# Performance work log

Hardware: AMD Instinct MI355X
Metric: run time of the kernel (lower is better)

## Reference

```python
import jax, jax.numpy as jnp
import numpy as np

B, TQ, TK, DQ, DK, DV = 16, 1024, 1024, 1024, 1024, 1024


def setup_inputs() -> dict:
    key = jax.random.key(0)
    k1, k2, k3, k4, k5 = jax.random.split(key, 5)
    query = jax.random.normal(k1, (B, TQ, DQ), dtype=jnp.float32)
    keys = jax.random.normal(k2, (B, TK, DK), dtype=jnp.float32)
    values = jax.random.normal(k3, (B, TK, DV), dtype=jnp.float32)
    W = jax.random.normal(k4, (DQ, DK), dtype=jnp.float32) / np.sqrt(DQ)
    mask = jax.random.normal(k5, (B, TK), dtype=jnp.float32)
    return {"query": query, "keys": keys, "values": values, "W": W, "mask": mask}


def reference(query, keys, values, W, mask):
    # Bilinear (Luong 'general') score: weight[b,q,k] = query[b,q,:] @ W @ keys[b,k,:]
    qW = jnp.einsum('bqd,de->bqe', query, W)              # [B, Tq, Dk]
    weight = jnp.einsum('bqe,bke->bqk', qW, keys)         # [B, Tq, Tk]
    weight = weight + mask[:, None, :]                    # additive mask, broadcast over Tq
    score = jax.nn.softmax(weight, axis=-1)               # [B, Tq, Tk]
    ctx = jnp.einsum('bqk,bkv->bqv', score, values)       # [B, Tq, Dv]
    return (score, ctx)
```

## Files before the change

### kernel.cpp

```cpp
#include <hip/hip_runtime.h>
#include <hip/hip_bf16.h>

typedef _Float16 f16;
typedef __attribute__((ext_vector_type(8))) _Float16 half8;
typedef __attribute__((ext_vector_type(4))) float f32x4;

#define BM 256
#define BN 256
#define BK 64

__device__ __forceinline__ void gl2lds16(const f16* g, const f16* l) {
    __builtin_amdgcn_global_load_lds(
        (const __attribute__((address_space(1))) unsigned int*)g,
        (__attribute__((address_space(3))) unsigned int*)l, 16, 0, 0);
}

#define MFMA(d, a, b) d = __builtin_amdgcn_mfma_f32_16x16x32_f16(a, b, d, 0, 0, 0)

__global__ __launch_bounds__(256)
void cast_f16(const float* __restrict__ in, f16* __restrict__ out, long long n) {
    long long i = ((long long)blockIdx.x * 256 + threadIdx.x) * 8;
    if (i >= n) return;
    float4 a = *(const float4*)&in[i];
    float4 b = *(const float4*)&in[i + 4];
    union { f16 h[8]; uint4 q; } H;
    H.h[0] = (f16)a.x; H.h[1] = (f16)a.y; H.h[2] = (f16)a.z; H.h[3] = (f16)a.w;
    H.h[4] = (f16)b.x; H.h[5] = (f16)b.y; H.h[6] = (f16)b.z; H.h[7] = (f16)b.w;
    *(uint4*)&out[i] = H.q;
}

__global__ __launch_bounds__(256)
void transpose_f16(const float* __restrict__ in, f16* __restrict__ out,
                   int R, int C, long long in_stride, long long out_stride) {
    const int b = blockIdx.z;
    in += (size_t)b * in_stride;
    out += (size_t)b * out_stride;

    __shared__ float tile[32][33];
    const int r0 = blockIdx.y * 32, c0 = blockIdx.x * 32;
    const int t = threadIdx.x;
    const int tr = t >> 5, tc = t & 31;
    for (int i = 0; i < 4; i++)
        tile[tr + i * 8][tc] = in[(size_t)(r0 + tr + i * 8) * C + c0 + tc];
    __syncthreads();
    for (int i = 0; i < 4; i++) {
        float v = tile[tc][tr + i * 8];
        out[(size_t)(c0 + tr + i * 8) * R + r0 + tc] = (f16)v;
    }
}

template<int EPI>
__global__ __launch_bounds__(512, 2)
void gemm256(const f16* __restrict__ A_, const f16* __restrict__ B_,
             float* __restrict__ Cf, f16* __restrict__ Ch,
             const float* __restrict__ mask,
             int M, int N, int K,
             long long batchA, long long batchB, long long batchC) {
    const int b = blockIdx.z;
    const int m0 = blockIdx.y * BM;
    const int n0 = blockIdx.x * BN;
    const int t = threadIdx.x;
    const int lane = t & 63, wv = t >> 6;
    const int wr = wv >> 2;
    const int wc = wv & 3;

    const f16* A = A_ + (size_t)b * batchA;
    const f16* B = B_ + (size_t)b * batchB;

    __shared__ alignas(16) f16 sA[2][2][128][64];
    __shared__ alignas(16) f16 sB[2][2][128][64];

    const int srow  = wv * 16 + (lane >> 3);
    const int gslot = (lane & 7) ^ (lane >> 3);

    const f16* gAl  = A + (size_t)(m0 + srow) * K + gslot * 8;
    const f16* gAl8 = gAl + (size_t)8 * K;
    const f16* gAh  = gAl + (size_t)128 * K;
    const f16* gAh8 = gAl8 + (size_t)128 * K;
    const f16* gBl  = B + (size_t)(n0 + srow) * K + gslot * 8;
    const f16* gBl8 = gBl + (size_t)8 * K;
    const f16* gBh  = gBl + (size_t)128 * K;
    const f16* gBh8 = gBl8 + (size_t)128 * K;

    f32x4 acc[8][4];
#pragma unroll
    for (int i = 0; i < 8; i++)
#pragma unroll
        for (int j = 0; j < 4; j++)
#pragma unroll
            for (int r = 0; r < 4; r++) acc[i][j][r] = 0.0f;

    gl2lds16(gAl,  &sA[0][0][wv * 16][0]); gl2lds16(gAl8, &sA[0][0][wv * 16 + 8][0]);
    gl2lds16(gAh,  &sA[0][1][wv * 16][0]); gl2lds16(gAh8, &sA[0][1][wv * 16 + 8][0]);
    gl2lds16(gBl,  &sB[0][0][wv * 16][0]); gl2lds16(gBl8, &sB[0][0][wv * 16 + 8][0]);
    gl2lds16(gBh,  &sB[0][1][wv * 16][0]); gl2lds16(gBh8, &sB[0][1][wv * 16 + 8][0]);

    const int fr  = lane & 15;
    const int fq4 = lane >> 4;
    const int NT  = K / BK;

    half8 af[4][2], bA[2][2], bB[2][2];

    for (int tt = 0; tt < NT; ++tt) {
        const int c = tt & 1, cn = c ^ 1;
        const size_t kg = (size_t)(tt + 1) * BK;
        const bool nx = (tt + 1 < NT);

        const f16* pa = &sA[c][wr][fr][0];
        const f16* pb = &sB[c][wc >> 1][(wc & 1) * 64 + fr][0];
        const int cs0 = ((0 + fq4) ^ (fr & 7)) * 8;
        const int cs1 = ((4 + fq4) ^ (fr & 7)) * 8;

        if (nx) {
            gl2lds16(gAl + kg,  &sA[cn][0][wv * 16][0]);
            gl2lds16(gAl8 + kg, &sA[cn][0][wv * 16 + 8][0]);
            asm volatile("s_waitcnt vmcnt(2)\n\ts_barrier" ::: "memory");
        } else {
            asm volatile("s_waitcnt vmcnt(0)\n\ts_barrier" ::: "memory");
        }
#pragma unroll
        for (int mi = 0; mi < 4; mi++) {
            af[mi][0] = *(const half8*)(pa + mi * 1024 + cs0);
            af[mi][1] = *(const half8*)(pa + mi * 1024 + cs1);
        }
#pragma unroll
        for (int ni = 0; ni < 2; ni++) {
            bA[ni][0] = *(const half8*)(pb + ni * 1024 + cs0);
            bA[ni][1] = *(const half8*)(pb + ni * 1024 + cs1);
        }
        __builtin_amdgcn_s_setprio(1);
#pragma unroll
        for (int mi = 0; mi < 4; mi++)
#pragma unroll
            for (int ni = 0; ni < 2; ni++) {
                MFMA(acc[mi][ni], af[mi][0], bA[ni][0]);
                MFMA(acc[mi][ni], af[mi][1], bA[ni][1]);
            }
        __builtin_amdgcn_s_setprio(0);

        if (nx) {
            gl2lds16(gAh + kg,  &sA[cn][1][wv * 16][0]);
            gl2lds16(gAh8 + kg, &sA[cn][1][wv * 16 + 8][0]);
        }
#pragma unroll
        for (int ni = 0; ni < 2; ni++) {
            bB[ni][0] = *(const half8*)(pb + (2 + ni) * 1024 + cs0);
            bB[ni][1] = *(const half8*)(pb + (2 + ni) * 1024 + cs1);
        }
        __builtin_amdgcn_s_setprio(1);
#pragma unroll
        for (int mi = 0; mi < 4; mi++)
#pragma unroll
            for (int ni = 0; ni < 2; ni++) {
                MFMA(acc[mi][2 + ni], af[mi][0], bB[ni][0]);
                MFMA(acc[mi][2 + ni], af[mi][1], bB[ni][1]);
            }
        __builtin_amdgcn_s_setprio(0);

        if (nx) {
            gl2lds16(gBl + kg,  &sB[cn][0][wv * 16][0]);
            gl2lds16(gBl8 + kg, &sB[cn][0][wv * 16 + 8][0]);
        }
#pragma unroll
        for (int mi = 0; mi < 4; mi++) {
            af[mi][0] = *(const half8*)(pa + (64 + mi * 16) * 64 + cs0);
            af[mi][1] = *(const half8*)(pa + (64 + mi * 16) * 64 + cs1);
        }
        __builtin_amdgcn_s_setprio(1);
#pragma unroll
        for (int mi = 0; mi < 4; mi++)
#pragma unroll
            for (int ni = 0; ni < 2; ni++) {
                MFMA(acc[4 + mi][2 + ni], af[mi][0], bB[ni][0]);
                MFMA(acc[4 + mi][2 + ni], af[mi][1], bB[ni][1]);
            }
        __builtin_amdgcn_s_setprio(0);

        if (nx) {
            gl2lds16(gBh + kg,  &sB[cn][1][wv * 16][0]);
            gl2lds16(gBh8 + kg, &sB[cn][1][wv * 16 + 8][0]);
        }
        __builtin_amdgcn_s_setprio(1);
#pragma unroll
        for (int mi = 0; mi < 4; mi++)
#pragma unroll
            for (int ni = 0; ni < 2; ni++) {
                MFMA(acc[4 + mi][ni], af[mi][0], bA[ni][0]);
                MFMA(acc[4 + mi][ni], af[mi][1], bA[ni][1]);
            }
        __builtin_amdgcn_s_setprio(0);
        asm volatile("s_barrier" ::: "memory");
    }

    const int q4 = (lane >> 4) * 4;
    float mv[4] = {0.f, 0.f, 0.f, 0.f};
    if constexpr (EPI == 1) {
#pragma unroll
        for (int ni = 0; ni < 4; ni++)
            mv[ni] = mask[(size_t)b * N + n0 + wc * 64 + ni * 16 + fr];
    }
#pragma unroll
    for (int mi = 0; mi < 8; mi++)
#pragma unroll
        for (int ni = 0; ni < 4; ni++) {
            const int col = n0 + wc * 64 + ni * 16 + fr;
#pragma unroll
            for (int r = 0; r < 4; r++) {
                const int row = m0 + wr * 128 + mi * 16 + q4 + r;
                const size_t idx = (size_t)b * batchC + (size_t)row * N + col;
                float v = acc[mi][ni][r];
                if constexpr (EPI == 0) {
                    Cf[idx] = v;
                } else if constexpr (EPI == 1) {
                    Cf[idx] = v + mv[ni];
                } else {
                    Ch[idx] = (f16)v;
                }
            }
        }
}

__global__ __launch_bounds__(256)
void softmax_rows(float* __restrict__ w, f16* __restrict__ sb) {
    const size_t row = blockIdx.x;
    float* p = w + row * 1024;
    const int t = threadIdx.x;
    const int wv = t >> 6, ln = t & 63;

    float4 v = *(const float4*)&p[t * 4];
    float m = fmaxf(fmaxf(v.x, v.y), fmaxf(v.z, v.w));
    for (int o = 32; o > 0; o >>= 1) m = fmaxf(m, __shfl_down(m, o));
    __shared__ float redm[4];
    if (ln == 0) redm[wv] = m;
    __syncthreads();
    m = fmaxf(fmaxf(redm[0], redm[1]), fmaxf(redm[2], redm[3]));

    float e0 = __expf(v.x - m), e1 = __expf(v.y - m);
    float e2 = __expf(v.z - m), e3 = __expf(v.w - m);
    float s = e0 + e1 + e2 + e3;
    for (int o = 32; o > 0; o >>= 1) s += __shfl_down(s, o);
    __shared__ float reds[4];
    if (ln == 0) reds[wv] = s;
    __syncthreads();
    s = reds[0] + reds[1] + reds[2] + reds[3];
    const float inv = 1.0f / s;

    float4 o4; o4.x = e0 * inv; o4.y = e1 * inv; o4.z = e2 * inv; o4.w = e3 * inv;
    *(float4*)&p[t * 4] = o4;
    union { f16 h[4]; uint2 q; } H;
    H.h[0] = (f16)o4.x; H.h[1] = (f16)o4.y; H.h[2] = (f16)o4.z; H.h[3] = (f16)o4.w;
    *(uint2*)&sb[row * 1024 + t * 4] = H.q;
}

extern "C" void kernel_launch(void* const* d_in, const int* in_sizes, int n_in,
                              void* d_out, int out_size, void* d_ws, size_t ws_size,
                              hipStream_t stream) {
    const int B = 16, T = 1024, D = 1024;
    const long long MAT = (long long)T * D;
    const long long BT = (long long)B * MAT;

    const float* query  = (const float*)d_in[0];
    const float* keys   = (const float*)d_in[1];
    const float* values = (const float*)d_in[2];
    const float* W      = (const float*)d_in[3];
    const float* mask   = (const float*)d_in[4];

    float* out = (float*)d_out;
    float* score_f = out;
    float* ctx_f   = out + (size_t)BT;

    char* ws = (char*)d_ws;
    f16* R1  = (f16*)ws;                   ws += (size_t)BT * 2;
    f16* R2  = (f16*)ws;                   ws += (size_t)BT * 2;
    f16* qw  = (f16*)ws;                   ws += (size_t)BT * 2;
    f16* wt  = (f16*)ws;                   ws += (size_t)MAT * 2;

    f16* qf = R1, *vt = R1;
    f16* kf = R2, *sc = R2;

    dim3 blk(256);
    dim3 blk5(512);

    cast_f16<<<dim3((unsigned)(BT / 2048)), blk, 0, stream>>>(query, qf, BT);
    transpose_f16<<<dim3(32, 32, 1), blk, 0, stream>>>(W, wt, D, D, 0, 0);

    gemm256<2><<<dim3(4, 64, 1), blk5, 0, stream>>>(
        qf, wt, nullptr, qw, nullptr, B * T, D, D, 0, 0, 0);

    cast_f16<<<dim3((unsigned)(BT / 2048)), blk, 0, stream>>>(keys, kf, BT);

    gemm256<1><<<dim3(4, 4, B), blk5, 0, stream>>>(
        qw, kf, score_f, nullptr, mask, T, T, D, MAT, MAT, MAT);

    transpose_f16<<<dim3(32, 32, B), blk, 0, stream>>>(values, vt, T, D, MAT, MAT);

    softmax_rows<<<B * T, blk, 0, stream>>>(score_f, sc);

    gemm256<0><<<dim3(4, 4, B), blk5, 0, stream>>>(
        sc, vt, ctx_f, nullptr, nullptr, T, D, T, MAT, MAT, MAT);
}
```

Measured before the change: 426.5 us.

## Fuse score GEMM with mask and softmax, widen transpose, remap blocks per XCD

Replaces the separate score GEMM plus row-softmax pass with one kernel in which each block computes a 64x1024 strip of scores, adds the mask, and performs the row max/sum reductions in registers and LDS before writing fp32 scores and f16 probabilities. This removes the round trip of the fp32 score matrix through global memory. The change also widens the transpose to 64x64 tiles with vectorized loads and stores, remaps the context GEMM's blocks so each XCD works on contiguous batches for L2 locality, and hoists a B-fragment LDS load earlier in the main GEMM loop. The fused kernel uses a 64-row tile and a large LDS buffer, so it may reach lower MFMA efficiency and occupancy than the 256x256 GEMM it replaces.

After: 421.8 us. About the same (-1.1%).

```diff
diff --git a/kernel.cpp b/kernel.cpp
--- a/kernel.cpp
+++ b/kernel.cpp
@@ -30,35 +30,52 @@
 }
 
 __global__ __launch_bounds__(256)
-void transpose_f16(const float* __restrict__ in, f16* __restrict__ out,
-                   int R, int C, long long in_stride, long long out_stride) {
+void transpose64_f16(const float* __restrict__ in, f16* __restrict__ out,
+                     int R, int C, long long in_stride, long long out_stride) {
     const int b = blockIdx.z;
     in += (size_t)b * in_stride;
     out += (size_t)b * out_stride;
 
-    __shared__ float tile[32][33];
-    const int r0 = blockIdx.y * 32, c0 = blockIdx.x * 32;
+    __shared__ float tile[64][68];
+    const int c0 = blockIdx.x * 64, r0 = blockIdx.y * 64;
     const int t = threadIdx.x;
-    const int tr = t >> 5, tc = t & 31;
-    for (int i = 0; i < 4; i++)
-        tile[tr + i * 8][tc] = in[(size_t)(r0 + tr + i * 8) * C + c0 + tc];
+
+    const int lr = t >> 4, lc4 = (t & 15) * 4;
+#pragma unroll
+    for (int p = 0; p < 4; p++) {
+        float4 v = *(const float4*)&in[(size_t)(r0 + p * 16 + lr) * C + c0 + lc4];
+        *(float4*)&tile[p * 16 + lr][lc4] = v;
+    }
     __syncthreads();
-    for (int i = 0; i < 4; i++) {
-        float v = tile[tc][tr + i * 8];
-        out[(size_t)(c0 + tr + i * 8) * R + r0 + tc] = (f16)v;
-    }
-}
-
-template<int EPI>
+
+    const int oc_ = t >> 3, rr = (t & 7) * 8;
+#pragma unroll
+    for (int p = 0; p < 2; p++) {
+        const int oc = p * 32 + oc_;
+        union { f16 h[8]; uint4 q; } H;
+#pragma unroll
+        for (int i = 0; i < 8; i++) H.h[i] = (f16)tile[rr + i][oc];
+        *(uint4*)&out[(size_t)(c0 + oc) * R + r0 + rr] = H.q;
+    }
+}
+
+template<int EPI, int XR>
 __global__ __launch_bounds__(512, 2)
 void gemm256(const f16* __restrict__ A_, const f16* __restrict__ B_,
              float* __restrict__ Cf, f16* __restrict__ Ch,
-             const float* __restrict__ mask,
              int M, int N, int K,
              long long batchA, long long batchB, long long batchC) {
-    const int b = blockIdx.z;
-    const int m0 = blockIdx.y * BM;
-    const int n0 = blockIdx.x * BN;
+    int bx, by, bz;
+    if constexpr (XR == 1) {
+        const int d = blockIdx.z * 16 + blockIdx.y * 4 + blockIdx.x;
+        const int xcd = d & 7, j = d >> 3, i2 = j & 15;
+        bz = xcd + 8 * (j >> 4); by = i2 >> 2; bx = i2 & 3;
+    } else {
+        bx = blockIdx.x; by = blockIdx.y; bz = blockIdx.z;
+    }
+    const int b = bz;
+    const int m0 = by * BM;
+    const int n0 = bx * BN;
     const int t = threadIdx.x;
     const int lane = t & 63, wv = t >> 6;
     const int wr = wv >> 2;
@@ -128,6 +145,11 @@
             bA[ni][0] = *(const half8*)(pb + ni * 1024 + cs0);
             bA[ni][1] = *(const half8*)(pb + ni * 1024 + cs1);
         }
+#pragma unroll
+        for (int ni = 0; ni < 2; ni++) {
+            bB[ni][0] = *(const half8*)(pb + (2 + ni) * 1024 + cs0);
+            bB[ni][1] = *(const half8*)(pb + (2 + ni) * 1024 + cs1);
+        }
         __builtin_amdgcn_s_setprio(1);
 #pragma unroll
         for (int mi = 0; mi < 4; mi++)
@@ -142,11 +164,6 @@
             gl2lds16(gAh + kg,  &sA[cn][1][wv * 16][0]);
             gl2lds16(gAh8 + kg, &sA[cn][1][wv * 16 + 8][0]);
         }
-#pragma unroll
-        for (int ni = 0; ni < 2; ni++) {
-            bB[ni][0] = *(const half8*)(pb + (2 + ni) * 1024 + cs0);
-            bB[ni][1] = *(const half8*)(pb + (2 + ni) * 1024 + cs1);
-        }
         __builtin_amdgcn_s_setprio(1);
 #pragma unroll
         for (int mi = 0; mi < 4; mi++)
@@ -193,12 +210,6 @@
     }
 
     const int q4 = (lane >> 4) * 4;
-    float mv[4] = {0.f, 0.f, 0.f, 0.f};
-    if constexpr (EPI == 1) {
-#pragma unroll
-        for (int ni = 0; ni < 4; ni++)
-            mv[ni] = mask[(size_t)b * N + n0 + wc * 64 + ni * 16 + fr];
-    }
 #pragma unroll
     for (int mi = 0; mi < 8; mi++)
 #pragma unroll
@@ -209,47 +220,199 @@
                 const int row = m0 + wr * 128 + mi * 16 + q4 + r;
                 const size_t idx = (size_t)b * batchC + (size_t)row * N + col;
                 float v = acc[mi][ni][r];
-                if constexpr (EPI == 0) {
-                    Cf[idx] = v;
-                } else if constexpr (EPI == 1) {
-                    Cf[idx] = v + mv[ni];
-                } else {
-                    Ch[idx] = (f16)v;
-                }
-            }
-        }
-}
-
-__global__ __launch_bounds__(256)
-void softmax_rows(float* __restrict__ w, f16* __restrict__ sb) {
-    const size_t row = blockIdx.x;
-    float* p = w + row * 1024;
+                if constexpr (EPI == 0) Cf[idx] = v;
+                else                    Ch[idx] = (f16)v;
+            }
+        }
+}
+
+__global__ __launch_bounds__(512, 2)
+void gemm_softmax(const f16* __restrict__ A_, const f16* __restrict__ B_,
+                  const float* __restrict__ mask,
+                  float* __restrict__ score, f16* __restrict__ sc,
+                  int N, int K, long long MAT) {
+    const int d = blockIdx.z * 16 + blockIdx.y;
+    const int xcd = d & 7, j = d >> 3;
+    const int b = xcd + 8 * (j >> 4);
+    const int m0 = (j & 15) * 64;
+
     const int t = threadIdx.x;
-    const int wv = t >> 6, ln = t & 63;
-
-    float4 v = *(const float4*)&p[t * 4];
-    float m = fmaxf(fmaxf(v.x, v.y), fmaxf(v.z, v.w));
-    for (int o = 32; o > 0; o >>= 1) m = fmaxf(m, __shfl_down(m, o));
-    __shared__ float redm[4];
-    if (ln == 0) redm[wv] = m;
+    const int lane = t & 63, wv = t >> 6;
+    const int fr = lane & 15;
+
+    const f16* A = A_ + (size_t)b * MAT;
+    const f16* B = B_ + (size_t)b * MAT;
+
+    __shared__ alignas(16) f16 sA2[2][64][32];
+    __shared__ alignas(16) f16 sB2[2][1024][32];
+    __shared__ float sRed[8][64];
+    __shared__ float sRed2[64];
+
+    const int brow = lane >> 2;
+    const int gsl  = (lane & 3) ^ ((lane >> 2) & 3);
+    const f16* gB = B + (size_t)(wv * 128 + brow) * K + gsl * 8;
+    const f16* gA = A + (size_t)(m0 + wv * 8 + brow) * K + gsl * 8;
+
+    f32x4 acc[4][8];
+#pragma unroll
+    for (int mi = 0; mi < 4; mi++)
+#pragma unroll
+        for (int ni = 0; ni < 8; ni++)
+#pragma unroll
+            for (int r = 0; r < 4; r++) acc[mi][ni][r] = 0.0f;
+
+#pragma unroll
+    for (int i = 0; i < 8; i++)
+        gl2lds16(gB + (size_t)i * 16 * K, &sB2[0][wv * 128 + i * 16][0]);
+    if (lane < 32) gl2lds16(gA, &sA2[0][wv * 8][0]);
+
+    const int NT = K / 32;
+    half8 afr[4], bfr[8];
+
+    for (int tt = 0; tt < NT; ++tt) {
+        const int c = tt & 1, cn = c ^ 1;
+        const size_t kg = (size_t)(tt + 1) * 32;
+        const bool nx = (tt + 1 < NT);
+
+        if (nx) {
+#pragma unroll
+            for (int i = 0; i < 8; i++)
+                gl2lds16(gB + (size_t)i * 16 * K + kg, &sB2[cn][wv * 128 + i * 16][0]);
+            if (lane < 32) gl2lds16(gA + kg, &sA2[cn][wv * 8][0]);
+            asm volatile("s_waitcnt vmcnt(9)\n\ts_barrier" ::: "memory");
+        } else {
+            asm volatile("s_waitcnt vmcnt(0)\n\ts_barrier" ::: "memory");
+        }
+
+        const int sl = ((lane >> 4) ^ (fr & 3)) * 8;
+#pragma unroll
+        for (int mi = 0; mi < 4; mi++)
+            afr[mi] = *(const half8*)&sA2[c][mi * 16 + fr][sl];
+#pragma unroll
+        for (int ni = 0; ni < 8; ni++)
+            bfr[ni] = *(const half8*)&sB2[c][wv * 128 + ni * 16 + fr][sl];
+
+        __builtin_amdgcn_s_setprio(1);
+#pragma unroll
+        for (int ni = 0; ni < 8; ni++)
+#pragma unroll
+            for (int mi = 0; mi < 4; mi++)
+                MFMA(acc[mi][ni], afr[mi], bfr[ni]);
+        __builtin_amdgcn_s_setprio(0);
+
+        asm volatile("s_barrier" ::: "memory");
+    }
+
+    const int q4 = (lane >> 4) * 4;
+
+    float mv[8];
+#pragma unroll
+    for (int ni = 0; ni < 8; ni++)
+        mv[ni] = mask[(size_t)b * N + wv * 128 + ni * 16 + fr];
+#pragma unroll
+    for (int mi = 0; mi < 4; mi++)
+#pragma unroll
+        for (int ni = 0; ni < 8; ni++)
+#pragma unroll
+            for (int r = 0; r < 4; r++) acc[mi][ni][r] += mv[ni];
+
+    float pm[4][4];
+#pragma unroll
+    for (int mi = 0; mi < 4; mi++)
+#pragma unroll
+        for (int r = 0; r < 4; r++) {
+            float x = acc[mi][0][r];
+#pragma unroll
+            for (int ni = 1; ni < 8; ni++) x = fmaxf(x, acc[mi][ni][r]);
+            pm[mi][r] = x;
+        }
+#pragma unroll
+    for (int o = 1; o < 16; o <<= 1)
+#pragma unroll
+        for (int mi = 0; mi < 4; mi++)
+#pragma unroll
+            for (int r = 0; r < 4; r++)
+                pm[mi][r] = fmaxf(pm[mi][r], __shfl_xor(pm[mi][r], o));
+
+    if (fr == 0)
+#pragma unroll
+        for (int mi = 0; mi < 4; mi++)
+#pragma unroll
+            for (int r = 0; r < 4; r++)
+                sRed[wv][mi * 16 + q4 + r] = pm[mi][r];
     __syncthreads();
-    m = fmaxf(fmaxf(redm[0], redm[1]), fmaxf(redm[2], redm[3]));
-
-    float e0 = __expf(v.x - m), e1 = __expf(v.y - m);
-    float e2 = __expf(v.z - m), e3 = __expf(v.w - m);
-    float s = e0 + e1 + e2 + e3;
-    for (int o = 32; o > 0; o >>= 1) s += __shfl_down(s, o);
-    __shared__ float reds[4];
-    if (ln == 0) reds[wv] = s;
+    if (t < 64) {
+        float x = sRed[0][t];
+#pragma unroll
+        for (int w = 1; w < 8; w++) x = fmaxf(x, sRed[w][t]);
+        sRed2[t] = x;
+    }
     __syncthreads();
-    s = reds[0] + reds[1] + reds[2] + reds[3];
-    const float inv = 1.0f / s;
-
-    float4 o4; o4.x = e0 * inv; o4.y = e1 * inv; o4.z = e2 * inv; o4.w = e3 * inv;
-    *(float4*)&p[t * 4] = o4;
-    union { f16 h[4]; uint2 q; } H;
-    H.h[0] = (f16)o4.x; H.h[1] = (f16)o4.y; H.h[2] = (f16)o4.z; H.h[3] = (f16)o4.w;
-    *(uint2*)&sb[row * 1024 + t * 4] = H.q;
+
+    float m_[4][4];
+#pragma unroll
+    for (int mi = 0; mi < 4; mi++)
+#pragma unroll
+        for (int r = 0; r < 4; r++) m_[mi][r] = sRed2[mi * 16 + q4 + r];
+
+    float ps[4][4];
+#pragma unroll
+    for (int mi = 0; mi < 4; mi++)
+#pragma unroll
+        for (int r = 0; r < 4; r++) ps[mi][r] = 0.0f;
+#pragma unroll
+    for (int mi = 0; mi < 4; mi++)
+#pragma unroll
+        for (int ni = 0; ni < 8; ni++)
+#pragma unroll
+            for (int r = 0; r < 4; r++) {
+                float e = __expf(acc[mi][ni][r] - m_[mi][r]);
+                acc[mi][ni][r] = e;
+                ps[mi][r] += e;
+            }
+#pragma unroll
+    for (int o = 1; o < 16; o <<= 1)
+#pragma unroll
+        for (int mi = 0; mi < 4; mi++)
+#pragma unroll
+            for (int r = 0; r < 4; r++)
+                ps[mi][r] += __shfl_xor(ps[mi][r], o);
+
+    if (fr == 0)
+#pragma unroll
+        for (int mi = 0; mi < 4; mi++)
+#pragma unroll
+            for (int r = 0; r < 4; r++)
+                sRed[wv][mi * 16 + q4 + r] = ps[mi][r];
+    __syncthreads();
+    if (t < 64) {
+        float x = sRed[0][t];
+#pragma unroll
+        for (int w = 1; w < 8; w++) x += sRed[w][t];
+        sRed2[t] = x;
+    }
+    __syncthreads();
+
+    float inv[4][4];
+#pragma unroll
+    for (int mi = 0; mi < 4; mi++)
+#pragma unroll
+        for (int r = 0; r < 4; r++) inv[mi][r] = 1.0f / sRed2[mi * 16 + q4 + r];
+
+#pragma unroll
+    for (int mi = 0; mi < 4; mi++)
+#pragma unroll
+        for (int ni = 0; ni < 8; ni++) {
+            const int col = wv * 128 + ni * 16 + fr;
+#pragma unroll
+            for (int r = 0; r < 4; r++) {
+                const int row = m0 + mi * 16 + q4 + r;
+                const size_t idx = (size_t)b * MAT + (size_t)row * N + col;
+                float v = acc[mi][ni][r] * inv[mi][r];
+                score[idx] = v;
+                sc[idx] = (f16)v;
+            }
+        }
 }
 
 extern "C" void kernel_launch(void* const* d_in, const int* in_sizes, int n_in,
@@ -272,30 +435,29 @@
     char* ws = (char*)d_ws;
     f16* R1  = (f16*)ws;                   ws += (size_t)BT * 2;
     f16* R2  = (f16*)ws;                   ws += (size_t)BT * 2;
-    f16* qw  = (f16*)ws;                   ws += (size_t)BT * 2;
+    f16* R3  = (f16*)ws;                   ws += (size_t)BT * 2;
     f16* wt  = (f16*)ws;                   ws += (size_t)MAT * 2;
 
-    f16* qf = R1, *vt = R1;
-    f16* kf = R2, *sc = R2;
+    f16* qf = R1, *sc = R1;
+    f16* kf = R2;
+    f16* qw = R3, *vt = R3;
 
     dim3 blk(256);
     dim3 blk5(512);
 
     cast_f16<<<dim3((unsigned)(BT / 2048)), blk, 0, stream>>>(query, qf, BT);
-    transpose_f16<<<dim3(32, 32, 1), blk, 0, stream>>>(W, wt, D, D, 0, 0);
-
-    gemm256<2><<<dim3(4, 64, 1), blk5, 0, stream>>>(
-        qf, wt, nullptr, qw, nullptr, B * T, D, D, 0, 0, 0);
+    transpose64_f16<<<dim3(16, 16, 1), blk, 0, stream>>>(W, wt, D, D, 0, 0);
+
+    gemm256<2, 0><<<dim3(4, 64, 1), blk5, 0, stream>>>(
+        qf, wt, nullptr, qw, B * T, D, D, 0, 0, 0);
 
     cast_f16<<<dim3((unsigned)(BT / 2048)), blk, 0, stream>>>(keys, kf, BT);
 
-    gemm256<1><<<dim3(4, 4, B), blk5, 0, stream>>>(
-        qw, kf, score_f, nullptr, mask, T, T, D, MAT, MAT, MAT);
-
-    transpose_f16<<<dim3(32, 32, B), blk, 0, stream>>>(values, vt, T, D, MAT, MAT);
-
-    softmax_rows<<<B * T, blk, 0, stream>>>(score_f, sc);
-
-    gemm256<0><<<dim3(4, 4, B), blk5, 0, stream>>>(
-        sc, vt, ctx_f, nullptr, nullptr, T, D, T, MAT, MAT, MAT);
-}
+    gemm_softmax<<<dim3(1, 16, B), blk5, 0, stream>>>(
+        qw, kf, mask, score_f, sc, T, D, MAT);
+
+    transpose64_f16<<<dim3(16, 16, B), blk, 0, stream>>>(values, vt, T, D, MAT, MAT);
+
+    gemm256<0, 1><<<dim3(4, 4, B), blk5, 0, stream>>>(
+        sc, vt, ctx_f, nullptr, T, D, T, MAT, MAT, MAT);
+}
```
